# Performance work log

Hardware: AMD Instinct MI355X
Metric: run time of the kernel (lower is better)

Reference implementation:

```python
import jax, jax.numpy as jnp
import numpy as np

B, S, QD = 4, 2048, 1024
NH, KVH, DH = 16, 4, 64
WIN = 256  # sliding_window


def setup_inputs() -> dict:
    key = jax.random.key(0)
    ks = jax.random.split(key, 5)
    s = QD ** -0.5
    return {
        "hidden_states": jax.random.normal(ks[0], (B, S, QD), jnp.float32),
        "Wq": jax.random.normal(ks[1], (QD, NH * DH), jnp.float32) * s,
        "Wk": jax.random.normal(ks[2], (QD, KVH * DH), jnp.float32) * s,
        "Wv": jax.random.normal(ks[3], (QD, KVH * DH), jnp.float32) * s,
        "Wo": jax.random.normal(ks[4], (NH * DH, QD), jnp.float32) * s,
    }


def reference(hidden_states, Wq, Wk, Wv, Wo):
    x = hidden_states
    # QKV projections (torch Linear, no bias)
    q = (x @ Wq).reshape(B, S, NH, DH).transpose(0, 2, 1, 3)    # [B,NH,S,DH]
    k = (x @ Wk).reshape(B, S, KVH, DH).transpose(0, 2, 1, 3)   # [B,KVH,S,DH]
    v = (x @ Wv).reshape(B, S, KVH, DH).transpose(0, 2, 1, 3)
    # GQA: instead of repeat_interleave on k/v, group query heads per kv head
    g = NH // KVH
    qg = q.reshape(B, KVH, g, S, DH)
    scale = DH ** -0.5
    scores = jnp.einsum('bkgsd,bktd->bkgst', qg, k) * scale      # [B,KVH,g,S,S]
    # Sliding-window mask: torch SDPA treats a FLOAT mask as ADDITIVE, and the
    # original builds a 0/1 float mask (1 where |i-j| <= window). Faithful: add it.
    idx = jnp.arange(S)
    win = (jnp.abs(idx[:, None] - idx[None, :]) <= WIN).astype(scores.dtype)  # [S,S]
    scores = scores + win  # broadcast over B,KVH,g (same mask for all batch/heads)
    attn = jax.nn.softmax(scores, axis=-1)
    out = jnp.einsum('bkgst,bktd->bkgsd', attn, v)               # [B,KVH,g,S,DH]
    out = out.reshape(B, NH, S, DH).transpose(0, 2, 1, 3).reshape(B, S, NH * DH)
    return out @ Wo
```

## Files before the change

### kernel.cpp

```cpp
#include <hip/hip_runtime.h>
#include <hip/hip_bf16.h>


using short8 = __attribute__((ext_vector_type(8))) short;
using f32x4  = __attribute__((ext_vector_type(4))) float;
using f32x16 = __attribute__((ext_vector_type(16))) float;
using uint2v = __attribute__((ext_vector_type(2))) unsigned int;

#define GLDS(g, l) __builtin_amdgcn_global_load_lds( \
    (const __attribute__((address_space(1))) void*)(g), \
    (__attribute__((address_space(3))) void*)(l), 16, 0, 0)

__device__ __forceinline__ unsigned short f2bf(float f) {
  union { float f; unsigned u; } v; v.f = f;
  unsigned r = v.u + 0x7fffu + ((v.u >> 16) & 1u);
  return (unsigned short)(r >> 16);
}

__device__ __forceinline__ unsigned cvtpk(float lo, float hi) {
  unsigned r;
  asm("v_cvt_pk_bf16_f32 %0, %1, %2" : "=v"(r) : "v"(lo), "v"(hi));
  return r;
}

__global__ void cvt_x_kernel(const float* __restrict__ X, unsigned short* __restrict__ Xb) {
  int i = (blockIdx.x * blockDim.x + threadIdx.x) * 4;
  float4 v = *reinterpret_cast<const float4*>(X + i);
  ushort4 o;
  o.x = f2bf(v.x); o.y = f2bf(v.y); o.z = f2bf(v.z); o.w = f2bf(v.w);
  *reinterpret_cast<ushort4*>(Xb + i) = o;
}

__global__ void tr_cvt_kernel(const float* __restrict__ src, unsigned short* __restrict__ dst, int C) {
  int idx = blockIdx.x * blockDim.x + threadIdx.x;
  int c = idx >> 10, r = idx & 1023;
  dst[idx] = f2bf(src[(size_t)r * C + c]);
}

template<int MODE>
__global__ __launch_bounds__(256) void gemm_bt_kernel(
    const unsigned short* __restrict__ A, const unsigned short* __restrict__ Bt,
    unsigned short* __restrict__ Qo, unsigned short* __restrict__ Ko,
    unsigned short* __restrict__ Vto, float* __restrict__ Co)
{
  __shared__ __align__(16) unsigned short As[128 * 32];
  __shared__ __align__(16) unsigned short Bs[128 * 32];
  const int m0 = blockIdx.x * 128;
  const int n0 = blockIdx.y * 128;
  const int t = threadIdx.x;
  const int w = t >> 6, l = t & 63;
  const int wr = w >> 1, wc = w & 1;

  f32x4 acc[4][4] = {};

  const size_t aoff = (size_t)(m0 + w * 16 + (l >> 2)) * 1024 + (size_t)((l & 3) * 8);
  const size_t boff = (size_t)(n0 + w * 16 + (l >> 2)) * 1024 + (size_t)((l & 3) * 8);

  for (int kt = 0; kt < 1024; kt += 32) {
    GLDS(A  + aoff + kt,             &As[w * 512]);
    GLDS(A  + aoff + 64 * 1024 + kt, &As[(w + 4) * 512]);
    GLDS(Bt + boff + kt,             &Bs[w * 512]);
    GLDS(Bt + boff + 64 * 1024 + kt, &Bs[(w + 4) * 512]);
    __syncthreads();

    short8 af[4], bfr[4];
#pragma unroll
    for (int mi = 0; mi < 4; ++mi) {
      int row = wr * 64 + mi * 16 + (l & 15);
      af[mi] = *reinterpret_cast<const short8*>(&As[row * 32 + (l >> 4) * 8]);
    }
#pragma unroll
    for (int ni = 0; ni < 4; ++ni) {
      int row = wc * 64 + ni * 16 + (l & 15);
      bfr[ni] = *reinterpret_cast<const short8*>(&Bs[row * 32 + (l >> 4) * 8]);
    }
#pragma unroll
    for (int mi = 0; mi < 4; ++mi)
#pragma unroll
      for (int ni = 0; ni < 4; ++ni)
        acc[mi][ni] = __builtin_amdgcn_mfma_f32_16x16x32_bf16(af[mi], bfr[ni], acc[mi][ni], 0, 0, 0);
    __syncthreads();
  }

#pragma unroll
  for (int mi = 0; mi < 4; ++mi)
#pragma unroll
    for (int ni = 0; ni < 4; ++ni)
#pragma unroll
      for (int r = 0; r < 4; ++r) {
        int m = m0 + wr * 64 + mi * 16 + (l >> 4) * 4 + r;
        int n = n0 + wc * 64 + ni * 16 + (l & 15);
        float val = acc[mi][ni][r];
        if (MODE == 0) {
          int b = m >> 11, s = m & 2047;
          unsigned short bv = f2bf(val);
          int T = s >> 5;
          if (n < 1024) {
            int h = n >> 6, d = n & 63;
            size_t base = ((((size_t)(b * 16 + h)) * 64 + T) * 4 + (d >> 4)) * 512;
            Qo[base + ((d >> 3) & 1) * 256 + (s & 31) * 8 + (d & 7)] = bv;
          } else if (n < 1280) {
            int kvh = (n - 1024) >> 6, d = n & 63;
            size_t base = ((((size_t)(b * 4 + kvh)) * 64 + T) * 4 + (d >> 4)) * 512;
            Ko[base + ((d >> 3) & 1) * 256 + (s & 31) * 8 + (d & 7)] = bv;
          } else {
            int kvh = (n - 1280) >> 6, d = n & 63;
            size_t base = ((((size_t)(b * 4 + kvh)) * 64 + T) * 4 +
                           ((d >> 5) * 2 + ((s >> 4) & 1))) * 512;
            Vto[base + ((s >> 3) & 1) * 256 + (d & 31) * 8 + (s & 7)] = bv;
          }
        } else {
          Co[((size_t)m << 10) + n] = val;
        }
      }
}

__global__ __launch_bounds__(256, 4) void attn_kernel(
    const unsigned short* __restrict__ Qf, const unsigned short* __restrict__ Kf,
    const unsigned short* __restrict__ Vf, unsigned short* __restrict__ AO)
{
  const int t = threadIdx.x, w = t >> 6, l = t & 63;
  const int hi = l >> 5, ln = l & 31;

  const int orig = blockIdx.x;
  const int swz = (orig & 7) * 128 + (orig >> 3);
  const int hf = swz >> 4;
  const int qt = swz & 15;
  const int b = hf >> 4, h = hf & 15, kvh = h >> 2;
  const int q0 = qt * 128 + w * 32;
  const int qrow = q0 + ln;

  const unsigned short* Qp = Qf + (((size_t)hf * 64 + qt * 4 + w) * 4) * 512;
  const unsigned short* Kt = Kf + ((size_t)(b * 4 + kvh) * 256) * 512 + l * 8;
  const unsigned short* Vt = Vf + ((size_t)(b * 4 + kvh) * 256) * 512 + l * 8;

  short8 qf[4];
#pragma unroll
  for (int kk = 0; kk < 4; ++kk)
    qf[kk] = *reinterpret_cast<const short8*>(Qp + kk * 512 + l * 8);

  f32x16 oA = {}, oB = {};
  float lsum = 0.f;
  const float C1  = 0.125f * 1.44269504f;
  const float L2E = 1.44269504f;
  const float FM  = 12.0f;

  for (int T = 0; T < 64; ++T) {
    short8 kf0 = *reinterpret_cast<const short8*>(Kt);
    short8 kf1 = *reinterpret_cast<const short8*>(Kt + 512);
    short8 kf2 = *reinterpret_cast<const short8*>(Kt + 1024);
    short8 kf3 = *reinterpret_cast<const short8*>(Kt + 1536);
    f32x16 s = {};
    s = __builtin_amdgcn_mfma_f32_32x32x16_bf16(kf0, qf[0], s, 0, 0, 0);
    s = __builtin_amdgcn_mfma_f32_32x32x16_bf16(kf1, qf[1], s, 0, 0, 0);
    s = __builtin_amdgcn_mfma_f32_32x32x16_bf16(kf2, qf[2], s, 0, 0, 0);
    s = __builtin_amdgcn_mfma_f32_32x32x16_bf16(kf3, qf[3], s, 0, 0, 0);
    short8 vf0 = *reinterpret_cast<const short8*>(Vt);
    short8 vf1 = *reinterpret_cast<const short8*>(Vt + 512);
    short8 vf2 = *reinterpret_cast<const short8*>(Vt + 1024);
    short8 vf3 = *reinterpret_cast<const short8*>(Vt + 1536);
    Kt += 2048; Vt += 2048;

    const int kv0 = T * 32;
    const int d = q0 - kv0;
    float p[16];
    if (d == 256 || d == -256) {
      const int qmb = qrow - kv0 - 4 * hi;
#pragma unroll
      for (int r = 0; r < 16; ++r) {
        const int kc = (r & 3) + 8 * (r >> 2);
        int df = qmb - kc; df = df < 0 ? -df : df;
        p[r] = __builtin_amdgcn_exp2f(
            __builtin_fmaf(s[r], C1, (df <= 256 ? L2E : 0.f) - FM));
      }
    } else {
      const float cc = ((d <= 224 && d >= -224) ? L2E : 0.f) - FM;
#pragma unroll
      for (int i = 0; i < 16; ++i)
        p[i] = __builtin_amdgcn_exp2f(__builtin_fmaf(s[i], C1, cc));
    }

    float s8[8], s4[4];
#pragma unroll
    for (int i = 0; i < 8; ++i) s8[i] = p[i] + p[i + 8];
#pragma unroll
    for (int i = 0; i < 4; ++i) s4[i] = s8[i] + s8[i + 4];
    float sum = (s4[0] + s4[1]) + (s4[2] + s4[3]);
    {
      uint2v sw = __builtin_amdgcn_permlane32_swap(__float_as_uint(sum), __float_as_uint(sum), false, false);
      sum = __uint_as_float(sw[0]) + __uint_as_float(sw[1]);
    }
    lsum += sum;

#pragma unroll
    for (int ks = 0; ks < 2; ++ks) {
      unsigned a0 = cvtpk(p[ks * 8 + 0], p[ks * 8 + 1]);
      unsigned a1 = cvtpk(p[ks * 8 + 2], p[ks * 8 + 3]);
      unsigned b0 = cvtpk(p[ks * 8 + 4], p[ks * 8 + 5]);
      unsigned b1 = cvtpk(p[ks * 8 + 6], p[ks * 8 + 7]);
      uint2v s0 = __builtin_amdgcn_permlane32_swap(a0, b0, false, false);
      uint2v s1 = __builtin_amdgcn_permlane32_swap(a1, b1, false, false);
      union { unsigned u[4]; short8 v; } pf;
      pf.u[0] = s0[0]; pf.u[1] = s1[0]; pf.u[2] = s0[1]; pf.u[3] = s1[1];
      oA = __builtin_amdgcn_mfma_f32_32x32x16_bf16(ks ? vf1 : vf0, pf.v, oA, 0, 0, 0);
      oB = __builtin_amdgcn_mfma_f32_32x32x16_bf16(ks ? vf3 : vf2, pf.v, oB, 0, 0, 0);
    }
  }

  const float inv = 1.f / lsum;
  unsigned short* Op = AO + ((size_t)(b * 2048 + qrow)) * 1024 + h * 64;
#pragma unroll
  for (int qd = 0; qd < 4; ++qd) {
    uint2 wv;
    wv.x = cvtpk(oA[4 * qd + 0] * inv, oA[4 * qd + 1] * inv);
    wv.y = cvtpk(oA[4 * qd + 2] * inv, oA[4 * qd + 3] * inv);
    *reinterpret_cast<uint2*>(Op + qd * 8 + hi * 4) = wv;
  }
#pragma unroll
  for (int qd = 0; qd < 4; ++qd) {
    uint2 wv;
    wv.x = cvtpk(oB[4 * qd + 0] * inv, oB[4 * qd + 1] * inv);
    wv.y = cvtpk(oB[4 * qd + 2] * inv, oB[4 * qd + 3] * inv);
    *reinterpret_cast<uint2*>(Op + 32 + qd * 8 + hi * 4) = wv;
  }
}

extern "C" void kernel_launch(void* const* d_in, const int* in_sizes, int n_in,
                              void* d_out, int out_size, void* d_ws, size_t ws_size,
                              hipStream_t stream)
{
  const float* X  = (const float*)d_in[0];
  const float* Wq = (const float*)d_in[1];
  const float* Wk = (const float*)d_in[2];
  const float* Wv = (const float*)d_in[3];
  const float* Wo = (const float*)d_in[4];
  float* out = (float*)d_out;
  char* ws = (char*)d_ws;

  unsigned short* Xb    = (unsigned short*)(ws);
  unsigned short* WqkvT = (unsigned short*)(ws + 16777216);
  unsigned short* WoT   = (unsigned short*)(ws + 19922944);
  unsigned short* Q     = (unsigned short*)(ws + 22020096);
  unsigned short* Kc    = (unsigned short*)(ws + 38797312);
  unsigned short* Vt    = (unsigned short*)(ws + 42991616);
  unsigned short* AO    = (unsigned short*)(ws + 47185920);

  cvt_x_kernel<<<8192, 256, 0, stream>>>(X, Xb);
  tr_cvt_kernel<<<4096, 256, 0, stream>>>(Wq, WqkvT, 1024);
  tr_cvt_kernel<<<1024, 256, 0, stream>>>(Wk, WqkvT + 1024 * 1024, 256);
  tr_cvt_kernel<<<1024, 256, 0, stream>>>(Wv, WqkvT + 1280 * 1024, 256);
  tr_cvt_kernel<<<4096, 256, 0, stream>>>(Wo, WoT, 1024);

  gemm_bt_kernel<0><<<dim3(64, 12), 256, 0, stream>>>(Xb, WqkvT, Q, Kc, Vt, nullptr);
  attn_kernel<<<1024, 256, 0, stream>>>(Q, Kc, Vt, AO);
  gemm_bt_kernel<1><<<dim3(64, 8), 256, 0, stream>>>(AO, WoT, nullptr, nullptr, nullptr, out);
}
```

Before: 196.7 us.

## Tile weight transpose in LDS and vectorize QKV GEMM epilogue stores

Replaces four per-element strided transpose-convert launches with one LDS-tiled transpose kernel that reads and writes coalesced. The QKV GEMM epilogue is reworked: for Q/K the MFMA operands are swapped so each lane holds four consecutive head-dim values and writes them packed as one 8-byte store. V gets its own launch (MODE 2) that writes four consecutive tokens into the transposed V layout as 8-byte stores. This cuts scattered 2-byte global stores and launch count, at the cost of an extra GEMM launch with only 128 blocks for V.

```diff
diff --git a/kernel.cpp b/kernel.cpp
--- a/kernel.cpp
+++ b/kernel.cpp
@@ -31,10 +31,30 @@
   *reinterpret_cast<ushort4*>(Xb + i) = o;
 }
 
-__global__ void tr_cvt_kernel(const float* __restrict__ src, unsigned short* __restrict__ dst, int C) {
-  int idx = blockIdx.x * blockDim.x + threadIdx.x;
-  int c = idx >> 10, r = idx & 1023;
-  dst[idx] = f2bf(src[(size_t)r * C + c]);
+__global__ __launch_bounds__(256) void wtr_kernel(
+    const float* __restrict__ Wq, const float* __restrict__ Wk,
+    const float* __restrict__ Wv, const float* __restrict__ Wo,
+    unsigned short* __restrict__ WqkvT, unsigned short* __restrict__ WoT)
+{
+  __shared__ float tile[32][33];
+  const int bx = blockIdx.x;
+  const int by = blockIdx.y;
+  const float* src; unsigned short* dst; int C, ct;
+  if (by < 32)      { src = Wq; dst = WqkvT;               C = 1024; ct = by; }
+  else if (by < 40) { src = Wk; dst = WqkvT + 1024 * 1024; C = 256;  ct = by - 32; }
+  else if (by < 48) { src = Wv; dst = WqkvT + 1280 * 1024; C = 256;  ct = by - 40; }
+  else              { src = Wo; dst = WoT;                 C = 1024; ct = by - 48; }
+  const int tx = threadIdx.x & 31, ty = threadIdx.x >> 5;
+  const int c0 = ct * 32, r0 = bx * 32;
+#pragma unroll
+  for (int i = 0; i < 4; ++i)
+    tile[ty + i * 8][tx] = src[(size_t)(r0 + ty + i * 8) * C + c0 + tx];
+  __syncthreads();
+#pragma unroll
+  for (int i = 0; i < 4; ++i) {
+    int c = ty + i * 8;
+    dst[(size_t)(c0 + c) * 1024 + r0 + tx] = f2bf(tile[tx][c]);
+  }
 }
 
 template<int MODE>
@@ -46,7 +66,7 @@
   __shared__ __align__(16) unsigned short As[128 * 32];
   __shared__ __align__(16) unsigned short Bs[128 * 32];
   const int m0 = blockIdx.x * 128;
-  const int n0 = blockIdx.y * 128;
+  const int n0 = (MODE == 2 ? 1280 : 0) + blockIdx.y * 128;
   const int t = threadIdx.x;
   const int w = t >> 6, l = t & 63;
   const int wr = w >> 1, wc = w & 1;
@@ -77,42 +97,70 @@
 #pragma unroll
     for (int mi = 0; mi < 4; ++mi)
 #pragma unroll
+      for (int ni = 0; ni < 4; ++ni) {
+        if (MODE == 0)
+          acc[mi][ni] = __builtin_amdgcn_mfma_f32_16x16x32_bf16(bfr[ni], af[mi], acc[mi][ni], 0, 0, 0);
+        else
+          acc[mi][ni] = __builtin_amdgcn_mfma_f32_16x16x32_bf16(af[mi], bfr[ni], acc[mi][ni], 0, 0, 0);
+      }
+    __syncthreads();
+  }
+
+  const int lo = (l >> 4) * 4;
+
+  if (MODE == 0) {
+#pragma unroll
+    for (int mi = 0; mi < 4; ++mi) {
+      const int tok = m0 + wr * 64 + mi * 16 + (l & 15);
+      const int bb = tok >> 11, ss = tok & 2047;
+      const size_t bT = (size_t)bb * 16, T5 = ss >> 5, q5 = ss & 31;
+#pragma unroll
+      for (int ni = 0; ni < 4; ++ni) {
+        const int ddb = n0 + wc * 64 + ni * 16;
+        uint2 wv;
+        wv.x = cvtpk(acc[mi][ni][0], acc[mi][ni][1]);
+        wv.y = cvtpk(acc[mi][ni][2], acc[mi][ni][3]);
+        size_t base; unsigned short* dstp;
+        if (ddb < 1024) {
+          int hh = ddb >> 6, kk = (ddb >> 4) & 3;
+          base = ((((size_t)(bb * 16 + hh)) * 64 + T5) * 4 + kk) * 512; dstp = Qo;
+        } else {
+          int kvh = (ddb - 1024) >> 6, kk = (ddb >> 4) & 3;
+          base = ((((size_t)(bb * 4 + kvh)) * 64 + T5) * 4 + kk) * 512; dstp = Ko;
+        }
+        *reinterpret_cast<uint2*>(dstp + base + (lo >> 3) * 256 + q5 * 8 + (lo & 7)) = wv;
+      }
+    }
+  } else if (MODE == 2) {
+#pragma unroll
+    for (int ni = 0; ni < 4; ++ni) {
+      const int dd = n0 + wc * 64 + ni * 16 + (l & 15);
+      const int kvh = (dd - 1280) >> 6, d6 = dd & 63;
+#pragma unroll
+      for (int mi = 0; mi < 4; ++mi) {
+        const int tokb = m0 + wr * 64 + mi * 16 + lo;
+        const int bb = tokb >> 11, ss = tokb & 2047;
+        const int T5 = ss >> 5;
+        const int f = (d6 >> 5) * 2 + (mi & 1);
+        uint2 wv;
+        wv.x = cvtpk(acc[mi][ni][0], acc[mi][ni][1]);
+        wv.y = cvtpk(acc[mi][ni][2], acc[mi][ni][3]);
+        size_t base = ((((size_t)(bb * 4 + kvh)) * 64 + T5) * 4 + f) * 512;
+        *reinterpret_cast<uint2*>(Vto + base + ((lo >> 3) & 1) * 256 + (d6 & 31) * 8 + (lo & 7)) = wv;
+      }
+    }
+  } else {
+#pragma unroll
+    for (int mi = 0; mi < 4; ++mi)
+#pragma unroll
       for (int ni = 0; ni < 4; ++ni)
-        acc[mi][ni] = __builtin_amdgcn_mfma_f32_16x16x32_bf16(af[mi], bfr[ni], acc[mi][ni], 0, 0, 0);
-    __syncthreads();
-  }
-
-#pragma unroll
-  for (int mi = 0; mi < 4; ++mi)
-#pragma unroll
-    for (int ni = 0; ni < 4; ++ni)
-#pragma unroll
-      for (int r = 0; r < 4; ++r) {
-        int m = m0 + wr * 64 + mi * 16 + (l >> 4) * 4 + r;
-        int n = n0 + wc * 64 + ni * 16 + (l & 15);
-        float val = acc[mi][ni][r];
-        if (MODE == 0) {
-          int b = m >> 11, s = m & 2047;
-          unsigned short bv = f2bf(val);
-          int T = s >> 5;
-          if (n < 1024) {
-            int h = n >> 6, d = n & 63;
-            size_t base = ((((size_t)(b * 16 + h)) * 64 + T) * 4 + (d >> 4)) * 512;
-            Qo[base + ((d >> 3) & 1) * 256 + (s & 31) * 8 + (d & 7)] = bv;
-          } else if (n < 1280) {
-            int kvh = (n - 1024) >> 6, d = n & 63;
-            size_t base = ((((size_t)(b * 4 + kvh)) * 64 + T) * 4 + (d >> 4)) * 512;
-            Ko[base + ((d >> 3) & 1) * 256 + (s & 31) * 8 + (d & 7)] = bv;
-          } else {
-            int kvh = (n - 1280) >> 6, d = n & 63;
-            size_t base = ((((size_t)(b * 4 + kvh)) * 64 + T) * 4 +
-                           ((d >> 5) * 2 + ((s >> 4) & 1))) * 512;
-            Vto[base + ((s >> 3) & 1) * 256 + (d & 31) * 8 + (s & 7)] = bv;
-          }
-        } else {
-          Co[((size_t)m << 10) + n] = val;
+#pragma unroll
+        for (int r = 0; r < 4; ++r) {
+          int m = m0 + wr * 64 + mi * 16 + lo + r;
+          int n = n0 + wc * 64 + ni * 16 + (l & 15);
+          Co[((size_t)m << 10) + n] = acc[mi][ni][r];
         }
-      }
+  }
 }
 
 __global__ __launch_bounds__(256, 4) void attn_kernel(
@@ -246,12 +294,10 @@
   unsigned short* AO    = (unsigned short*)(ws + 47185920);
 
   cvt_x_kernel<<<8192, 256, 0, stream>>>(X, Xb);
-  tr_cvt_kernel<<<4096, 256, 0, stream>>>(Wq, WqkvT, 1024);
-  tr_cvt_kernel<<<1024, 256, 0, stream>>>(Wk, WqkvT + 1024 * 1024, 256);
-  tr_cvt_kernel<<<1024, 256, 0, stream>>>(Wv, WqkvT + 1280 * 1024, 256);
-  tr_cvt_kernel<<<4096, 256, 0, stream>>>(Wo, WoT, 1024);
-
-  gemm_bt_kernel<0><<<dim3(64, 12), 256, 0, stream>>>(Xb, WqkvT, Q, Kc, Vt, nullptr);
+  wtr_kernel<<<dim3(32, 80), 256, 0, stream>>>(Wq, Wk, Wv, Wo, WqkvT, WoT);
+
+  gemm_bt_kernel<0><<<dim3(64, 10), 256, 0, stream>>>(Xb, WqkvT, Q, Kc, nullptr, nullptr);
+  gemm_bt_kernel<2><<<dim3(64, 2),  256, 0, stream>>>(Xb, WqkvT, nullptr, nullptr, Vt, nullptr);
   attn_kernel<<<1024, 256, 0, stream>>>(Q, Kc, Vt, AO);
-  gemm_bt_kernel<1><<<dim3(64, 8), 256, 0, stream>>>(AO, WoT, nullptr, nullptr, nullptr, out);
-}
+  gemm_bt_kernel<1><<<dim3(64, 8),  256, 0, stream>>>(AO, WoT, nullptr, nullptr, nullptr, out);
+}
```

Measured after the change: 200.8 us. 1.02x slower.
